# Optimization experiments

Hardware: AMD Instinct MI355X
Metric: run time of the kernel (lower is better)

Reference implementation:

```python
import jax, jax.numpy as jnp
import numpy as np


def sparsemax(z):
    # Sparsemax along last axis: Euclidean projection of z onto the simplex.
    S = z.shape[-1]
    z_sorted = jnp.flip(jnp.sort(z, axis=-1), axis=-1)          # descending
    cssv = jnp.cumsum(z_sorted, axis=-1)                         # cumulative sums
    r = jnp.arange(1, S + 1, dtype=z.dtype)                      # 1..S
    support = 1.0 + r * z_sorted > cssv                          # support mask
    k = jnp.sum(support, axis=-1, keepdims=True)                 # support size (int)
    tau = (jnp.take_along_axis(cssv, k - 1, axis=-1) - 1.0) / k.astype(z.dtype)
    return jnp.maximum(z - tau, 0.0)


def setup_inputs() -> dict:
    key = jax.random.key(0)
    k1, k2, k3 = jax.random.split(key, 3)
    B, L, S, H, E, D = 8, 1024, 1024, 16, 64, 64
    queries = jax.random.normal(k1, (B, L, H, E), dtype=jnp.float32)
    keys = jax.random.normal(k2, (B, S, H, E), dtype=jnp.float32)
    values = jax.random.normal(k3, (B, S, H, D), dtype=jnp.float32)
    return {"queries": queries, "keys": keys, "values": values}


def reference(queries, keys, values):
    E = queries.shape[-1]
    scale = 1.0 / jnp.sqrt(jnp.asarray(E, dtype=queries.dtype))
    # [B,H,L,S] attention scores
    scores = jnp.einsum('blhe,bshe->bhls', queries, keys)
    A = sparsemax(scale * scores)                                # sparsemax normalization (dropout p=0)
    attn_output = jnp.einsum('bhls,bshd->blhd', A, values)
    return attn_output
```

## Files before the change

### kernel.cpp

```cpp
#include <hip/hip_runtime.h>


typedef _Float16 f16x8 __attribute__((ext_vector_type(8)));
typedef float    f32x4 __attribute__((ext_vector_type(4)));

constexpr int kB = 8, kL = 1024, kS = 1024, kH = 16, kE = 64, kD = 64;
constexpr int LT   = 32;
constexpr int JT   = 128;
constexpr int CAP  = 112;
constexpr int KMAX = CAP / 16;
constexpr int SUP  = 24;

__device__ __forceinline__ float pk2(float a, float b) {
  auto h = __builtin_amdgcn_cvt_pkrtz(a, b);
  return __builtin_bit_cast(float, h);
}

__device__ __forceinline__ float unpack_z(unsigned v) {
  return __uint_as_float((v & ~1023u) | 512u);
}

__global__ __launch_bounds__(512, 4)
void sparsemax_attn(const float* __restrict__ Q, const float* __restrict__ K,
                    const float* __restrict__ V, float* __restrict__ O) {
  __shared__ float4   Ksh[JT * 8];
  __shared__ float4   Qsh[LT * 8];
  __shared__ unsigned lists[LT * CAP];
  __shared__ unsigned sup_s[LT][SUP];
  __shared__ int      cnt_s[LT];
  __shared__ int      cnt2_s[LT];
  __shared__ float    rmax_s[LT][4];
  __shared__ float    tau_s[LT];

  const int t = threadIdx.x, lane = t & 63, w = t >> 6;
  const int qg = w >> 2, jg = w & 3;
  const int li = lane & 15, g = lane >> 4;
  const int myrow = qg * 16 + li;

  const int id  = blockIdx.x;
  const int xcd = id & 7, kk = id >> 3;
  const int bh  = xcd * 16 + (kk >> 5);
  const int b   = bh >> 4, h = bh & 15;
  const int l0  = (kk & 31) * LT;

  const float* Kbh = K + ((size_t)b * kS * kH + h) * kE;
  const float* Vb  = V + ((size_t)b * kS * kH + h) * kD;

  if (t < LT) { cnt_s[t] = 0; cnt2_s[t] = 0; }
  if (t >= 384 && t < 512) ((float*)rmax_s)[t - 384] = -1e30f;
  if (t < 256) {
    const int jj = t >> 3, e8 = t & 7;
    const float4* qp =
        (const float4*)(Q + (((size_t)(b * kL + l0 + jj)) * kH + h) * kE + e8 * 8);
    float4 q0 = qp[0], q1 = qp[1];
    q0.x *= .125f; q0.y *= .125f; q0.z *= .125f; q0.w *= .125f;
    q1.x *= .125f; q1.y *= .125f; q1.z *= .125f; q1.w *= .125f;
    Qsh[jj * 8 + (e8 ^ (jj & 7))] =
        make_float4(pk2(q0.x, q0.y), pk2(q0.z, q0.w), pk2(q1.x, q1.y), pk2(q1.z, q1.w));
  }

  float runl = -1e30f;
  f16x8 b0, b1;

  for (int jt = 0; jt < kS / JT; ++jt) {
    __syncthreads();
#pragma unroll
    for (int i = 0; i < 2; ++i) {
      const int idx = t + 512 * i, jj = idx >> 3, e8 = idx & 7;
      const float4* kp =
          (const float4*)(Kbh + (size_t)(jt * JT + jj) * (kH * kE) + e8 * 8);
      const float4 c0 = kp[0], c1 = kp[1];
      Ksh[jj * 8 + (e8 ^ (jj & 7))] =
          make_float4(pk2(c0.x, c0.y), pk2(c0.z, c0.w), pk2(c1.x, c1.y), pk2(c1.z, c1.w));
    }
    __syncthreads();
    if (jt == 0) {
      b0 = __builtin_bit_cast(f16x8, Qsh[myrow * 8 + ((0 + g) ^ (myrow & 7))]);
      b1 = __builtin_bit_cast(f16x8, Qsh[myrow * 8 + ((4 + g) ^ (myrow & 7))]);
    }

    f32x4 acc[2];
    acc[0] = f32x4{0.f, 0.f, 0.f, 0.f};
    acc[1] = f32x4{0.f, 0.f, 0.f, 0.f};
#pragma unroll
    for (int ct = 0; ct < 2; ++ct) {
      const int jl = jg * 32 + ct * 16 + li;
      const f16x8 a0 = __builtin_bit_cast(f16x8, Ksh[jl * 8 + ((0 + g) ^ (jl & 7))]);
      const f16x8 a1 = __builtin_bit_cast(f16x8, Ksh[jl * 8 + ((4 + g) ^ (jl & 7))]);
      acc[ct] = __builtin_amdgcn_mfma_f32_16x16x32_f16(a0, b0, acc[ct], 0, 0, 0);
      acc[ct] = __builtin_amdgcn_mfma_f32_16x16x32_f16(a1, b1, acc[ct], 0, 0, 0);
    }

    const float m01 = fmaxf(fmaxf(acc[0][0], acc[0][1]), fmaxf(acc[0][2], acc[0][3]));
    const float m23 = fmaxf(fmaxf(acc[1][0], acc[1][1]), fmaxf(acc[1][2], acc[1][3]));
    runl = fmaxf(runl, fmaxf(m01, m23));
    float mr = fmaxf(runl, __shfl_xor(runl, 16));
    mr = fmaxf(mr, __shfl_xor(mr, 32));
    if (lane < 16) rmax_s[myrow][jg] = mr;
    float rm = fmaxf(fmaxf(rmax_s[myrow][0], rmax_s[myrow][1]),
                     fmaxf(rmax_s[myrow][2], rmax_s[myrow][3]));
    const float thr = fmaxf(rm, mr) - 1.0f;
    const int jbase = jt * JT + jg * 32 + g * 4;
#pragma unroll
    for (int ct = 0; ct < 2; ++ct)
#pragma unroll
      for (int r = 0; r < 4; ++r) {
        const float z = acc[ct][r];
        if (z > thr) {
          const int pos = atomicAdd(&cnt_s[myrow], 1);
          if (pos < CAP)
            lists[myrow * CAP + pos] =
                (__float_as_uint(z) & ~1023u) | (unsigned)(jbase + ct * 16 + r);
        }
      }
  }
  __syncthreads();

  const int q0 = w * 4;
  {
    const int row = q0 + g;
    const int n   = cnt_s[row];
    const int nc  = min(n, CAP);
    float zr[KMAX];
#pragma unroll
    for (int k = 0; k < KMAX; ++k) {
      const int i = li + 16 * k;
      zr[k] = (i < nc) ? unpack_z(lists[row * CAP + i]) : -1e30f;
    }
    const float M =
        fmaxf(fmaxf(rmax_s[row][0], rmax_s[row][1]), fmaxf(rmax_s[row][2], rmax_s[row][3]));
    float t0 = M - 1.0f;
    for (int it = 0; it < 14; ++it) {
      float s = 0.f, c = 0.f;
#pragma unroll
      for (int k = 0; k < KMAX; ++k) {
        const float d = zr[k] - t0;
        if (d > 0.f) { s += d; c += 1.f; }
      }
      s += __shfl_xor(s, 1); c += __shfl_xor(c, 1);
      s += __shfl_xor(s, 2); c += __shfl_xor(c, 2);
      s += __shfl_xor(s, 4); c += __shfl_xor(c, 4);
      s += __shfl_xor(s, 8); c += __shfl_xor(c, 8);
      const float delta = (s - 1.0f) / fmaxf(c, 1.f);
      t0 += fmaxf(delta, 0.f);
      if (__all(delta <= 1e-6f)) break;
    }
    if (li == 0) tau_s[row] = t0;
#pragma unroll
    for (int k = 0; k < KMAX; ++k) {
      const int i = li + 16 * k;
      if (i < nc && zr[k] > t0) {
        const int pos = atomicAdd(&cnt2_s[row], 1);
        if (pos < SUP) sup_s[row][pos] = lists[row * CAP + i];
      }
    }
  }

#pragma unroll 1
  for (int r4 = 0; r4 < 4; ++r4) {
    const int row = q0 + r4;
    const int n   = cnt_s[row];
    const size_t obase = (((size_t)(b * kL + l0 + row)) * kH + h) * kD;
    if (n <= CAP) {
      const float tau = tau_s[row];
      const int k2 = cnt2_s[row];
      f32x4 o4 = {0.f, 0.f, 0.f, 0.f};
      if (k2 <= SUP) {
        for (int i = g; i < k2; i += 4) {
          const unsigned e = sup_s[row][i];
          const float  p = fmaxf(unpack_z(e) - tau, 0.f);
          const float4 v =
              ((const float4*)(Vb + (size_t)(e & 1023u) * (kH * kD)))[li];
          o4.x = fmaf(p, v.x, o4.x);
          o4.y = fmaf(p, v.y, o4.y);
          o4.z = fmaf(p, v.z, o4.z);
          o4.w = fmaf(p, v.w, o4.w);
        }
      } else {
        const int nc = n;
        for (int i = g; i < nc; i += 8) {
          const int   i2 = i + 4;
          const bool  ok2 = (i2 < nc);
          const unsigned e1 = lists[row * CAP + i];
          const unsigned e2 = lists[row * CAP + (ok2 ? i2 : i)];
          const float  p1 = fmaxf(unpack_z(e1) - tau, 0.f);
          const float  p2 = ok2 ? fmaxf(unpack_z(e2) - tau, 0.f) : 0.f;
          const float4 v1 =
              ((const float4*)(Vb + (size_t)(e1 & 1023u) * (kH * kD)))[li];
          const float4 v2 =
              ((const float4*)(Vb + (size_t)(e2 & 1023u) * (kH * kD)))[li];
          o4.x = fmaf(p1, v1.x, fmaf(p2, v2.x, o4.x));
          o4.y = fmaf(p1, v1.y, fmaf(p2, v2.y, o4.y));
          o4.z = fmaf(p1, v1.z, fmaf(p2, v2.z, o4.z));
          o4.w = fmaf(p1, v1.w, fmaf(p2, v2.w, o4.w));
        }
      }
      o4.x += __shfl_xor(o4.x, 16); o4.y += __shfl_xor(o4.y, 16);
      o4.z += __shfl_xor(o4.z, 16); o4.w += __shfl_xor(o4.w, 16);
      o4.x += __shfl_xor(o4.x, 32); o4.y += __shfl_xor(o4.y, 32);
      o4.z += __shfl_xor(o4.z, 32); o4.w += __shfl_xor(o4.w, 32);
      if (lane < 16)
        ((float4*)(O + obase))[li] = make_float4(o4.x, o4.y, o4.z, o4.w);
    } else {
      float scr2[16];
      for (int cc = 0; cc < 16; ++cc) {
        const int j = lane + 64 * cc;
        const float* kr = Kbh + (size_t)j * (kH * kE);
        float zz = 0.f;
        for (int e8 = 0; e8 < 8; ++e8) {
          const f16x8 qh = __builtin_bit_cast(f16x8, Qsh[row * 8 + (e8 ^ (row & 7))]);
          const float4* kp = (const float4*)(kr + e8 * 8);
          const float4 c0 = kp[0], c1 = kp[1];
          zz += (float)qh[0] * c0.x + (float)qh[1] * c0.y + (float)qh[2] * c0.z +
                (float)qh[3] * c0.w + (float)qh[4] * c1.x + (float)qh[5] * c1.y +
                (float)qh[6] * c1.z + (float)qh[7] * c1.w;
        }
        scr2[cc] = zz;
      }
      const float M2 =
          fmaxf(fmaxf(rmax_s[row][0], rmax_s[row][1]), fmaxf(rmax_s[row][2], rmax_s[row][3]));
      float t0 = M2 - 1.0f;
      for (int it = 0; it < 48; ++it) {
        float s = 0.f, c = 0.f;
        for (int cc = 0; cc < 16; ++cc) {
          const float d = scr2[cc] - t0;
          if (d > 0.f) { s += d; c += 1.f; }
        }
        for (int off = 32; off; off >>= 1) { s += __shfl_xor(s, off); c += __shfl_xor(c, off); }
        const float delta = (s - 1.0f) / fmaxf(c, 1.f);
        if (delta <= 1e-7f) break;
        t0 += delta;
      }
      float oacc = 0.f;
      for (int cc = 0; cc < 16; ++cc)
        for (int src = 0; src < 64; ++src) {
          const float z = __shfl(scr2[cc], src);
          const float p = z - t0;
          if (p > 0.f)
            oacc = fmaf(p, Vb[(size_t)(src + 64 * cc) * (kH * kD) + lane], oacc);
        }
      O[obase + lane] = oacc;
    }
  }
}

extern "C" void kernel_launch(void* const* d_in, const int* in_sizes, int n_in,
                              void* d_out, int out_size, void* d_ws, size_t ws_size,
                              hipStream_t stream) {
  (void)in_sizes; (void)n_in; (void)out_size; (void)d_ws; (void)ws_size;
  const float* Q = (const float*)d_in[0];
  const float* K = (const float*)d_in[1];
  const float* V = (const float*)d_in[2];
  float* O = (float*)d_out;
  sparsemax_attn<<<dim3(kB * kH * (kL / LT)), dim3(512), 0, stream>>>(Q, K, V, O);
}
```

Before: 412.6 us.

## Keep full K head resident in LDS and loop blocks over query chunks

Each block now loads the entire K matrix for one (batch, head) into shared memory once as fp16. It then iterates over 16 query chunks of 32 rows, covering half of L, instead of reloading K tiles for every 32-row query tile. This removes repeated global K loads and the per-tile syncs between K loads. In exchange, LDS use grows to about 128KB per block, occupancy is lowered (launch bounds 2), and the grid shrinks to 256 blocks, which may underfill the GPU and serialise work.

```diff
diff --git a/kernel.cpp b/kernel.cpp
--- a/kernel.cpp
+++ b/kernel.cpp
@@ -7,6 +7,7 @@
 constexpr int kB = 8, kL = 1024, kS = 1024, kH = 16, kE = 64, kD = 64;
 constexpr int LT   = 32;
 constexpr int JT   = 128;
+constexpr int NCH  = 16;
 constexpr int CAP  = 112;
 constexpr int KMAX = CAP / 16;
 constexpr int SUP  = 24;
@@ -20,10 +21,10 @@
   return __uint_as_float((v & ~1023u) | 512u);
 }
 
-__global__ __launch_bounds__(512, 4)
+__global__ __launch_bounds__(512, 2)
 void sparsemax_attn(const float* __restrict__ Q, const float* __restrict__ K,
                     const float* __restrict__ V, float* __restrict__ O) {
-  __shared__ float4   Ksh[JT * 8];
+  __shared__ float4   Ksh[kS * 8];
   __shared__ float4   Qsh[LT * 8];
   __shared__ unsigned lists[LT * CAP];
   __shared__ unsigned sup_s[LT][SUP];
@@ -38,208 +39,211 @@
   const int myrow = qg * 16 + li;
 
   const int id  = blockIdx.x;
-  const int xcd = id & 7, kk = id >> 3;
-  const int bh  = xcd * 16 + (kk >> 5);
+  const int bh  = id >> 1;
   const int b   = bh >> 4, h = bh & 15;
-  const int l0  = (kk & 31) * LT;
+  const int Lbase = (id & 1) * (kL / 2);
 
   const float* Kbh = K + ((size_t)b * kS * kH + h) * kE;
   const float* Vb  = V + ((size_t)b * kS * kH + h) * kD;
 
-  if (t < LT) { cnt_s[t] = 0; cnt2_s[t] = 0; }
-  if (t >= 384 && t < 512) ((float*)rmax_s)[t - 384] = -1e30f;
-  if (t < 256) {
-    const int jj = t >> 3, e8 = t & 7;
-    const float4* qp =
-        (const float4*)(Q + (((size_t)(b * kL + l0 + jj)) * kH + h) * kE + e8 * 8);
-    float4 q0 = qp[0], q1 = qp[1];
-    q0.x *= .125f; q0.y *= .125f; q0.z *= .125f; q0.w *= .125f;
-    q1.x *= .125f; q1.y *= .125f; q1.z *= .125f; q1.w *= .125f;
-    Qsh[jj * 8 + (e8 ^ (jj & 7))] =
-        make_float4(pk2(q0.x, q0.y), pk2(q0.z, q0.w), pk2(q1.x, q1.y), pk2(q1.z, q1.w));
+#pragma unroll
+  for (int u = 0; u < 16; ++u) {
+    const int idx = t + 512 * u, jj = idx >> 3, e8 = idx & 7;
+    const float4* kp = (const float4*)(Kbh + (size_t)jj * (kH * kE) + e8 * 8);
+    const float4 c0 = kp[0], c1 = kp[1];
+    Ksh[jj * 8 + (e8 ^ (jj & 7))] =
+        make_float4(pk2(c0.x, c0.y), pk2(c0.z, c0.w), pk2(c1.x, c1.y), pk2(c1.z, c1.w));
   }
 
-  float runl = -1e30f;
-  f16x8 b0, b1;
-
-  for (int jt = 0; jt < kS / JT; ++jt) {
+#pragma unroll 1
+  for (int c = 0; c < NCH; ++c) {
+    const int l0 = Lbase + c * LT;
     __syncthreads();
-#pragma unroll
-    for (int i = 0; i < 2; ++i) {
-      const int idx = t + 512 * i, jj = idx >> 3, e8 = idx & 7;
-      const float4* kp =
-          (const float4*)(Kbh + (size_t)(jt * JT + jj) * (kH * kE) + e8 * 8);
-      const float4 c0 = kp[0], c1 = kp[1];
-      Ksh[jj * 8 + (e8 ^ (jj & 7))] =
-          make_float4(pk2(c0.x, c0.y), pk2(c0.z, c0.w), pk2(c1.x, c1.y), pk2(c1.z, c1.w));
+
+    if (t < LT) { cnt_s[t] = 0; cnt2_s[t] = 0; }
+    if (t >= 384 && t < 512) ((float*)rmax_s)[t - 384] = -1e30f;
+    if (t < 256) {
+      const int jj = t >> 3, e8 = t & 7;
+      const float4* qp =
+          (const float4*)(Q + (((size_t)(b * kL + l0 + jj)) * kH + h) * kE + e8 * 8);
+      float4 q0 = qp[0], q1 = qp[1];
+      q0.x *= .125f; q0.y *= .125f; q0.z *= .125f; q0.w *= .125f;
+      q1.x *= .125f; q1.y *= .125f; q1.z *= .125f; q1.w *= .125f;
+      Qsh[jj * 8 + (e8 ^ (jj & 7))] =
+          make_float4(pk2(q0.x, q0.y), pk2(q0.z, q0.w), pk2(q1.x, q1.y), pk2(q1.z, q1.w));
     }
     __syncthreads();
-    if (jt == 0) {
-      b0 = __builtin_bit_cast(f16x8, Qsh[myrow * 8 + ((0 + g) ^ (myrow & 7))]);
-      b1 = __builtin_bit_cast(f16x8, Qsh[myrow * 8 + ((4 + g) ^ (myrow & 7))]);
-    }
-
-    f32x4 acc[2];
-    acc[0] = f32x4{0.f, 0.f, 0.f, 0.f};
-    acc[1] = f32x4{0.f, 0.f, 0.f, 0.f};
-#pragma unroll
-    for (int ct = 0; ct < 2; ++ct) {
-      const int jl = jg * 32 + ct * 16 + li;
-      const f16x8 a0 = __builtin_bit_cast(f16x8, Ksh[jl * 8 + ((0 + g) ^ (jl & 7))]);
-      const f16x8 a1 = __builtin_bit_cast(f16x8, Ksh[jl * 8 + ((4 + g) ^ (jl & 7))]);
-      acc[ct] = __builtin_amdgcn_mfma_f32_16x16x32_f16(a0, b0, acc[ct], 0, 0, 0);
-      acc[ct] = __builtin_amdgcn_mfma_f32_16x16x32_f16(a1, b1, acc[ct], 0, 0, 0);
-    }
-
-    const float m01 = fmaxf(fmaxf(acc[0][0], acc[0][1]), fmaxf(acc[0][2], acc[0][3]));
-    const float m23 = fmaxf(fmaxf(acc[1][0], acc[1][1]), fmaxf(acc[1][2], acc[1][3]));
-    runl = fmaxf(runl, fmaxf(m01, m23));
-    float mr = fmaxf(runl, __shfl_xor(runl, 16));
-    mr = fmaxf(mr, __shfl_xor(mr, 32));
-    if (lane < 16) rmax_s[myrow][jg] = mr;
-    float rm = fmaxf(fmaxf(rmax_s[myrow][0], rmax_s[myrow][1]),
-                     fmaxf(rmax_s[myrow][2], rmax_s[myrow][3]));
-    const float thr = fmaxf(rm, mr) - 1.0f;
-    const int jbase = jt * JT + jg * 32 + g * 4;
-#pragma unroll
-    for (int ct = 0; ct < 2; ++ct)
-#pragma unroll
-      for (int r = 0; r < 4; ++r) {
-        const float z = acc[ct][r];
-        if (z > thr) {
-          const int pos = atomicAdd(&cnt_s[myrow], 1);
-          if (pos < CAP)
-            lists[myrow * CAP + pos] =
-                (__float_as_uint(z) & ~1023u) | (unsigned)(jbase + ct * 16 + r);
-        }
-      }
-  }
-  __syncthreads();
-
-  const int q0 = w * 4;
-  {
-    const int row = q0 + g;
-    const int n   = cnt_s[row];
-    const int nc  = min(n, CAP);
-    float zr[KMAX];
-#pragma unroll
-    for (int k = 0; k < KMAX; ++k) {
-      const int i = li + 16 * k;
-      zr[k] = (i < nc) ? unpack_z(lists[row * CAP + i]) : -1e30f;
-    }
-    const float M =
-        fmaxf(fmaxf(rmax_s[row][0], rmax_s[row][1]), fmaxf(rmax_s[row][2], rmax_s[row][3]));
-    float t0 = M - 1.0f;
-    for (int it = 0; it < 14; ++it) {
-      float s = 0.f, c = 0.f;
+
+    const f16x8 b0 = __builtin_bit_cast(f16x8, Qsh[myrow * 8 + ((0 + g) ^ (myrow & 7))]);
+    const f16x8 b1 = __builtin_bit_cast(f16x8, Qsh[myrow * 8 + ((4 + g) ^ (myrow & 7))]);
+
+    float runl = -1e30f;
+
+#pragma unroll 1
+    for (int jt = 0; jt < kS / JT; ++jt) {
+      f32x4 acc[2];
+      acc[0] = f32x4{0.f, 0.f, 0.f, 0.f};
+      acc[1] = f32x4{0.f, 0.f, 0.f, 0.f};
+#pragma unroll
+      for (int ct = 0; ct < 2; ++ct) {
+        const int jrow = jg * 32 + ct * 16 + li;
+        const int jabs = jt * JT + jrow;
+        const f16x8 a0 = __builtin_bit_cast(f16x8, Ksh[jabs * 8 + ((0 + g) ^ (jrow & 7))]);
+        const f16x8 a1 = __builtin_bit_cast(f16x8, Ksh[jabs * 8 + ((4 + g) ^ (jrow & 7))]);
+        acc[ct] = __builtin_amdgcn_mfma_f32_16x16x32_f16(a0, b0, acc[ct], 0, 0, 0);
+        acc[ct] = __builtin_amdgcn_mfma_f32_16x16x32_f16(a1, b1, acc[ct], 0, 0, 0);
+      }
+
+      const float m01 = fmaxf(fmaxf(acc[0][0], acc[0][1]), fmaxf(acc[0][2], acc[0][3]));
+      const float m23 = fmaxf(fmaxf(acc[1][0], acc[1][1]), fmaxf(acc[1][2], acc[1][3]));
+      runl = fmaxf(runl, fmaxf(m01, m23));
+      float mr = fmaxf(runl, __shfl_xor(runl, 16));
+      mr = fmaxf(mr, __shfl_xor(mr, 32));
+      if (lane < 16) rmax_s[myrow][jg] = mr;
+      float rm = fmaxf(fmaxf(rmax_s[myrow][0], rmax_s[myrow][1]),
+                       fmaxf(rmax_s[myrow][2], rmax_s[myrow][3]));
+      const float thr = fmaxf(rm, mr) - 1.0f;
+      const int jbase = jt * JT + jg * 32 + g * 4;
+#pragma unroll
+      for (int ct = 0; ct < 2; ++ct)
+#pragma unroll
+        for (int r = 0; r < 4; ++r) {
+          const float z = acc[ct][r];
+          if (z > thr) {
+            const int pos = atomicAdd(&cnt_s[myrow], 1);
+            if (pos < CAP)
+              lists[myrow * CAP + pos] =
+                  (__float_as_uint(z) & ~1023u) | (unsigned)(jbase + ct * 16 + r);
+          }
+        }
+    }
+    __syncthreads();
+
+    const int q0 = w * 4;
+    {
+      const int row = q0 + g;
+      const int n   = cnt_s[row];
+      const int nc  = min(n, CAP);
+      float zr[KMAX];
 #pragma unroll
       for (int k = 0; k < KMAX; ++k) {
-        const float d = zr[k] - t0;
-        if (d > 0.f) { s += d; c += 1.f; }
-      }
-      s += __shfl_xor(s, 1); c += __shfl_xor(c, 1);
-      s += __shfl_xor(s, 2); c += __shfl_xor(c, 2);
-      s += __shfl_xor(s, 4); c += __shfl_xor(c, 4);
-      s += __shfl_xor(s, 8); c += __shfl_xor(c, 8);
-      const float delta = (s - 1.0f) / fmaxf(c, 1.f);
-      t0 += fmaxf(delta, 0.f);
-      if (__all(delta <= 1e-6f)) break;
-    }
-    if (li == 0) tau_s[row] = t0;
-#pragma unroll
-    for (int k = 0; k < KMAX; ++k) {
-      const int i = li + 16 * k;
-      if (i < nc && zr[k] > t0) {
-        const int pos = atomicAdd(&cnt2_s[row], 1);
-        if (pos < SUP) sup_s[row][pos] = lists[row * CAP + i];
-      }
-    }
-  }
+        const int i = li + 16 * k;
+        zr[k] = (i < nc) ? unpack_z(lists[row * CAP + i]) : -1e30f;
+      }
+      const float M =
+          fmaxf(fmaxf(rmax_s[row][0], rmax_s[row][1]), fmaxf(rmax_s[row][2], rmax_s[row][3]));
+      float t0 = M - 1.0f;
+      for (int it = 0; it < 14; ++it) {
+        float s = 0.f, cc = 0.f;
+#pragma unroll
+        for (int k = 0; k < KMAX; ++k) {
+          const float d = zr[k] - t0;
+          if (d > 0.f) { s += d; cc += 1.f; }
+        }
+        s += __shfl_xor(s, 1); cc += __shfl_xor(cc, 1);
+        s += __shfl_xor(s, 2); cc += __shfl_xor(cc, 2);
+        s += __shfl_xor(s, 4); cc += __shfl_xor(cc, 4);
+        s += __shfl_xor(s, 8); cc += __shfl_xor(cc, 8);
+        const float delta = (s - 1.0f) / fmaxf(cc, 1.f);
+        t0 += fmaxf(delta, 0.f);
+        if (__all(delta <= 1e-6f)) break;
+      }
+      if (li == 0) tau_s[row] = t0;
+#pragma unroll
+      for (int k = 0; k < KMAX; ++k) {
+        const int i = li + 16 * k;
+        if (i < nc && zr[k] > t0) {
+          const int pos = atomicAdd(&cnt2_s[row], 1);
+          if (pos < SUP) sup_s[row][pos] = lists[row * CAP + i];
+        }
+      }
+    }
 
 #pragma unroll 1
-  for (int r4 = 0; r4 < 4; ++r4) {
-    const int row = q0 + r4;
-    const int n   = cnt_s[row];
-    const size_t obase = (((size_t)(b * kL + l0 + row)) * kH + h) * kD;
-    if (n <= CAP) {
-      const float tau = tau_s[row];
-      const int k2 = cnt2_s[row];
-      f32x4 o4 = {0.f, 0.f, 0.f, 0.f};
-      if (k2 <= SUP) {
-        for (int i = g; i < k2; i += 4) {
-          const unsigned e = sup_s[row][i];
-          const float  p = fmaxf(unpack_z(e) - tau, 0.f);
-          const float4 v =
-              ((const float4*)(Vb + (size_t)(e & 1023u) * (kH * kD)))[li];
-          o4.x = fmaf(p, v.x, o4.x);
-          o4.y = fmaf(p, v.y, o4.y);
-          o4.z = fmaf(p, v.z, o4.z);
-          o4.w = fmaf(p, v.w, o4.w);
-        }
+    for (int r4 = 0; r4 < 4; ++r4) {
+      const int row = q0 + r4;
+      const int n   = cnt_s[row];
+      const size_t obase = (((size_t)(b * kL + l0 + row)) * kH + h) * kD;
+      if (n <= CAP) {
+        const float tau = tau_s[row];
+        const int k2 = cnt2_s[row];
+        f32x4 o4 = {0.f, 0.f, 0.f, 0.f};
+        if (k2 <= SUP) {
+          for (int i = g; i < k2; i += 4) {
+            const unsigned e = sup_s[row][i];
+            const float  p = fmaxf(unpack_z(e) - tau, 0.f);
+            const float4 v =
+                ((const float4*)(Vb + (size_t)(e & 1023u) * (kH * kD)))[li];
+            o4.x = fmaf(p, v.x, o4.x);
+            o4.y = fmaf(p, v.y, o4.y);
+            o4.z = fmaf(p, v.z, o4.z);
+            o4.w = fmaf(p, v.w, o4.w);
+          }
+        } else {
+          const int nc = n;
+          for (int i = g; i < nc; i += 8) {
+            const int   i2 = i + 4;
+            const bool  ok2 = (i2 < nc);
+            const unsigned e1 = lists[row * CAP + i];
+            const unsigned e2 = lists[row * CAP + (ok2 ? i2 : i)];
+            const float  p1 = fmaxf(unpack_z(e1) - tau, 0.f);
+            const float  p2 = ok2 ? fmaxf(unpack_z(e2) - tau, 0.f) : 0.f;
+            const float4 v1 =
+                ((const float4*)(Vb + (size_t)(e1 & 1023u) * (kH * kD)))[li];
+            const float4 v2 =
+                ((const float4*)(Vb + (size_t)(e2 & 1023u) * (kH * kD)))[li];
+            o4.x = fmaf(p1, v1.x, fmaf(p2, v2.x, o4.x));
+            o4.y = fmaf(p1, v1.y, fmaf(p2, v2.y, o4.y));
+            o4.z = fmaf(p1, v1.z, fmaf(p2, v2.z, o4.z));
+            o4.w = fmaf(p1, v1.w, fmaf(p2, v2.w, o4.w));
+          }
+        }
+        o4.x += __shfl_xor(o4.x, 16); o4.y += __shfl_xor(o4.y, 16);
+        o4.z += __shfl_xor(o4.z, 16); o4.w += __shfl_xor(o4.w, 16);
+        o4.x += __shfl_xor(o4.x, 32); o4.y += __shfl_xor(o4.y, 32);
+        o4.z += __shfl_xor(o4.z, 32); o4.w += __shfl_xor(o4.w, 32);
+        if (lane < 16)
+          ((float4*)(O + obase))[li] = make_float4(o4.x, o4.y, o4.z, o4.w);
       } else {
-        const int nc = n;
-        for (int i = g; i < nc; i += 8) {
-          const int   i2 = i + 4;
-          const bool  ok2 = (i2 < nc);
-          const unsigned e1 = lists[row * CAP + i];
-          const unsigned e2 = lists[row * CAP + (ok2 ? i2 : i)];
-          const float  p1 = fmaxf(unpack_z(e1) - tau, 0.f);
-          const float  p2 = ok2 ? fmaxf(unpack_z(e2) - tau, 0.f) : 0.f;
-          const float4 v1 =
-              ((const float4*)(Vb + (size_t)(e1 & 1023u) * (kH * kD)))[li];
-          const float4 v2 =
-              ((const float4*)(Vb + (size_t)(e2 & 1023u) * (kH * kD)))[li];
-          o4.x = fmaf(p1, v1.x, fmaf(p2, v2.x, o4.x));
-          o4.y = fmaf(p1, v1.y, fmaf(p2, v2.y, o4.y));
-          o4.z = fmaf(p1, v1.z, fmaf(p2, v2.z, o4.z));
-          o4.w = fmaf(p1, v1.w, fmaf(p2, v2.w, o4.w));
-        }
-      }
-      o4.x += __shfl_xor(o4.x, 16); o4.y += __shfl_xor(o4.y, 16);
-      o4.z += __shfl_xor(o4.z, 16); o4.w += __shfl_xor(o4.w, 16);
-      o4.x += __shfl_xor(o4.x, 32); o4.y += __shfl_xor(o4.y, 32);
-      o4.z += __shfl_xor(o4.z, 32); o4.w += __shfl_xor(o4.w, 32);
-      if (lane < 16)
-        ((float4*)(O + obase))[li] = make_float4(o4.x, o4.y, o4.z, o4.w);
-    } else {
-      float scr2[16];
-      for (int cc = 0; cc < 16; ++cc) {
-        const int j = lane + 64 * cc;
-        const float* kr = Kbh + (size_t)j * (kH * kE);
-        float zz = 0.f;
-        for (int e8 = 0; e8 < 8; ++e8) {
-          const f16x8 qh = __builtin_bit_cast(f16x8, Qsh[row * 8 + (e8 ^ (row & 7))]);
-          const float4* kp = (const float4*)(kr + e8 * 8);
-          const float4 c0 = kp[0], c1 = kp[1];
-          zz += (float)qh[0] * c0.x + (float)qh[1] * c0.y + (float)qh[2] * c0.z +
-                (float)qh[3] * c0.w + (float)qh[4] * c1.x + (float)qh[5] * c1.y +
-                (float)qh[6] * c1.z + (float)qh[7] * c1.w;
-        }
-        scr2[cc] = zz;
-      }
-      const float M2 =
-          fmaxf(fmaxf(rmax_s[row][0], rmax_s[row][1]), fmaxf(rmax_s[row][2], rmax_s[row][3]));
-      float t0 = M2 - 1.0f;
-      for (int it = 0; it < 48; ++it) {
-        float s = 0.f, c = 0.f;
+        float scr2[16];
         for (int cc = 0; cc < 16; ++cc) {
-          const float d = scr2[cc] - t0;
-          if (d > 0.f) { s += d; c += 1.f; }
-        }
-        for (int off = 32; off; off >>= 1) { s += __shfl_xor(s, off); c += __shfl_xor(c, off); }
-        const float delta = (s - 1.0f) / fmaxf(c, 1.f);
-        if (delta <= 1e-7f) break;
-        t0 += delta;
-      }
-      float oacc = 0.f;
-      for (int cc = 0; cc < 16; ++cc)
-        for (int src = 0; src < 64; ++src) {
-          const float z = __shfl(scr2[cc], src);
-          const float p = z - t0;
-          if (p > 0.f)
-            oacc = fmaf(p, Vb[(size_t)(src + 64 * cc) * (kH * kD) + lane], oacc);
-        }
-      O[obase + lane] = oacc;
+          const int j = lane + 64 * cc;
+          const float* kr = Kbh + (size_t)j * (kH * kE);
+          float zz = 0.f;
+          for (int e8 = 0; e8 < 8; ++e8) {
+            const f16x8 qh = __builtin_bit_cast(f16x8, Qsh[row * 8 + (e8 ^ (row & 7))]);
+            const float4* kp = (const float4*)(kr + e8 * 8);
+            const float4 c0 = kp[0], c1 = kp[1];
+            zz += (float)qh[0] * c0.x + (float)qh[1] * c0.y + (float)qh[2] * c0.z +
+                  (float)qh[3] * c0.w + (float)qh[4] * c1.x + (float)qh[5] * c1.y +
+                  (float)qh[6] * c1.z + (float)qh[7] * c1.w;
+          }
+          scr2[cc] = zz;
+        }
+        const float M2 =
+            fmaxf(fmaxf(rmax_s[row][0], rmax_s[row][1]), fmaxf(rmax_s[row][2], rmax_s[row][3]));
+        float t0 = M2 - 1.0f;
+        for (int it = 0; it < 48; ++it) {
+          float s = 0.f, cc2 = 0.f;
+          for (int cc = 0; cc < 16; ++cc) {
+            const float d = scr2[cc] - t0;
+            if (d > 0.f) { s += d; cc2 += 1.f; }
+          }
+          for (int off = 32; off; off >>= 1) { s += __shfl_xor(s, off); cc2 += __shfl_xor(cc2, off); }
+          const float delta = (s - 1.0f) / fmaxf(cc2, 1.f);
+          if (delta <= 1e-7f) break;
+          t0 += delta;
+        }
+        float oacc = 0.f;
+        for (int cc = 0; cc < 16; ++cc)
+          for (int src = 0; src < 64; ++src) {
+            const float z = __shfl(scr2[cc], src);
+            const float p = z - t0;
+            if (p > 0.f)
+              oacc = fmaf(p, Vb[(size_t)(src + 64 * cc) * (kH * kD) + lane], oacc);
+          }
+        O[obase + lane] = oacc;
+      }
     }
   }
 }
@@ -252,5 +256,5 @@
   const float* K = (const float*)d_in[1];
   const float* V = (const float*)d_in[2];
   float* O = (float*)d_out;
-  sparsemax_attn<<<dim3(kB * kH * (kL / LT)), dim3(512), 0, stream>>>(Q, K, V, O);
-}
+  sparsemax_attn<<<dim3(kB * kH * 2), dim3(512), 0, stream>>>(Q, K, V, O);
+}
```

Measured after the change: 682.4 us. 65.4% more time.

## Load K fragments directly from global into registers, drop shared K tile and barriers

Applied to the files above, without the earlier changes.

Removes the shared-memory K staging tile and the two per-iteration __syncthreads, so each lane loads its K fragment straight from global memory and converts it to fp16 before the MFMA. The row-max read from shared memory is moved to the top of the iteration, and the occupancy hint in launch_bounds goes from 4 to 6. This cuts LDS traffic and barrier stalls and frees LDS so more blocks can be resident. In exchange, global loads are less coalesced and are duplicated across the query-group waves, and the cross-wave threshold now reads possibly stale maxima. That is harmless, since a threshold that is too low only admits more candidates.

```diff
diff --git a/kernel.cpp b/kernel.cpp
--- a/kernel.cpp
+++ b/kernel.cpp
@@ -20,10 +20,16 @@
   return __uint_as_float((v & ~1023u) | 512u);
 }
 
-__global__ __launch_bounds__(512, 4)
+__device__ __forceinline__ f16x8 ldk8(const float* __restrict__ p) {
+  const float4 c0 = ((const float4*)p)[0], c1 = ((const float4*)p)[1];
+  const float4 r = make_float4(pk2(c0.x, c0.y), pk2(c0.z, c0.w),
+                               pk2(c1.x, c1.y), pk2(c1.z, c1.w));
+  return __builtin_bit_cast(f16x8, r);
+}
+
+__global__ __launch_bounds__(512, 6)
 void sparsemax_attn(const float* __restrict__ Q, const float* __restrict__ K,
                     const float* __restrict__ V, float* __restrict__ O) {
-  __shared__ float4   Ksh[JT * 8];
   __shared__ float4   Qsh[LT * 8];
   __shared__ unsigned lists[LT * CAP];
   __shared__ unsigned sup_s[LT][SUP];
@@ -58,35 +64,29 @@
     Qsh[jj * 8 + (e8 ^ (jj & 7))] =
         make_float4(pk2(q0.x, q0.y), pk2(q0.z, q0.w), pk2(q1.x, q1.y), pk2(q1.z, q1.w));
   }
+  __syncthreads();
+
+  const f16x8 b0 = __builtin_bit_cast(f16x8, Qsh[myrow * 8 + ((0 + g) ^ (myrow & 7))]);
+  const f16x8 b1 = __builtin_bit_cast(f16x8, Qsh[myrow * 8 + ((4 + g) ^ (myrow & 7))]);
+
+  const float* Klane = Kbh + (size_t)(jg * 32 + li) * (kH * kE) + g * 8;
 
   float runl = -1e30f;
-  f16x8 b0, b1;
-
+
+#pragma unroll 1
   for (int jt = 0; jt < kS / JT; ++jt) {
-    __syncthreads();
-#pragma unroll
-    for (int i = 0; i < 2; ++i) {
-      const int idx = t + 512 * i, jj = idx >> 3, e8 = idx & 7;
-      const float4* kp =
-          (const float4*)(Kbh + (size_t)(jt * JT + jj) * (kH * kE) + e8 * 8);
-      const float4 c0 = kp[0], c1 = kp[1];
-      Ksh[jj * 8 + (e8 ^ (jj & 7))] =
-          make_float4(pk2(c0.x, c0.y), pk2(c0.z, c0.w), pk2(c1.x, c1.y), pk2(c1.z, c1.w));
-    }
-    __syncthreads();
-    if (jt == 0) {
-      b0 = __builtin_bit_cast(f16x8, Qsh[myrow * 8 + ((0 + g) ^ (myrow & 7))]);
-      b1 = __builtin_bit_cast(f16x8, Qsh[myrow * 8 + ((4 + g) ^ (myrow & 7))]);
-    }
-
+    const float rm_st = fmaxf(fmaxf(rmax_s[myrow][0], rmax_s[myrow][1]),
+                              fmaxf(rmax_s[myrow][2], rmax_s[myrow][3]));
+
+    const float* kt = Klane + (size_t)jt * JT * (kH * kE);
     f32x4 acc[2];
     acc[0] = f32x4{0.f, 0.f, 0.f, 0.f};
     acc[1] = f32x4{0.f, 0.f, 0.f, 0.f};
 #pragma unroll
     for (int ct = 0; ct < 2; ++ct) {
-      const int jl = jg * 32 + ct * 16 + li;
-      const f16x8 a0 = __builtin_bit_cast(f16x8, Ksh[jl * 8 + ((0 + g) ^ (jl & 7))]);
-      const f16x8 a1 = __builtin_bit_cast(f16x8, Ksh[jl * 8 + ((4 + g) ^ (jl & 7))]);
+      const float* kr = kt + (size_t)ct * 16 * (kH * kE);
+      const f16x8 a0 = ldk8(kr);
+      const f16x8 a1 = ldk8(kr + 32);
       acc[ct] = __builtin_amdgcn_mfma_f32_16x16x32_f16(a0, b0, acc[ct], 0, 0, 0);
       acc[ct] = __builtin_amdgcn_mfma_f32_16x16x32_f16(a1, b1, acc[ct], 0, 0, 0);
     }
@@ -97,9 +97,7 @@
     float mr = fmaxf(runl, __shfl_xor(runl, 16));
     mr = fmaxf(mr, __shfl_xor(mr, 32));
     if (lane < 16) rmax_s[myrow][jg] = mr;
-    float rm = fmaxf(fmaxf(rmax_s[myrow][0], rmax_s[myrow][1]),
-                     fmaxf(rmax_s[myrow][2], rmax_s[myrow][3]));
-    const float thr = fmaxf(rm, mr) - 1.0f;
+    const float thr = fmaxf(rm_st, mr) - 1.0f;
     const int jbase = jt * JT + jg * 32 + g * 4;
 #pragma unroll
     for (int ct = 0; ct < 2; ++ct)
```

Result: slower. 643.7 us (+56.0%).
